# Optimization experiments

Hardware: AMD Instinct MI355X
Metric: run time of the kernel (lower is better)

Reference implementation:

```python
import jax, jax.numpy as jnp
import numpy as np


def setup_inputs() -> dict:
    key = jax.random.key(0)
    k1, k2, k3 = jax.random.split(key, 3)
    bs, S, d, C = 2, 196, 512, 1006
    imgFeaturemap = jax.random.normal(k1, (bs, S, d), dtype=jnp.float32)
    wordFeatures = jax.random.normal(k2, (C, d), dtype=jnp.float32)
    fc3_w = jax.random.normal(k3, (d, d), dtype=jnp.float32) * 0.02
    fc3_b = jnp.zeros((d,), dtype=jnp.float32)
    return {"imgFeaturemap": imgFeaturemap, "wordFeatures": wordFeatures,
            "fc3_w": fc3_w, "fc3_b": fc3_b}


def reference(imgFeaturemap, wordFeatures, fc3_w, fc3_b):
    # imgFeaturemap: (bs, S, d); wordFeatures: (C, d)
    # Broadcast multiply + tanh: (bs, S, C, d)
    t = jnp.tanh(imgFeaturemap[:, :, None, :] * wordFeatures[None, None, :, :])
    # Per-row Linear (PyTorch Linear: x @ W^T + b)
    feat = jnp.einsum('bscd,ed->bsce', t, fc3_w) + fc3_b
    # Softmax over spatial axis S (axis=1), independently per (class, channel)
    coef = jax.nn.softmax(feat, axis=1)
    # Softmax-weighted spatial pooling per class: (bs, C, d)
    semanticFeature = jnp.einsum('bsd,bscd->bcd', imgFeaturemap, coef)
    return semanticFeature
```

## Files before the change

### kernel.cpp

```cpp
#include <hip/hip_runtime.h>

using half8   = __attribute__((ext_vector_type(8))) _Float16;
using floatx4 = __attribute__((ext_vector_type(4))) float;

namespace {
constexpr int S = 196, D = 512, C = 1006;
constexpr int CB  = 8;
constexpr int TPB = 768;
constexpr int RS  = 64;
constexpr int NPASS  = 25;
constexpr int NCHUNK = 200;
constexpr float KTANH = 2.885390082f;
constexpr float LOG2E = 1.44269504f;


__device__ __forceinline__ int sw_off(int row, int seg) {
    return row * RS + ((seg ^ (row & 7)) << 3);
}

__device__ __forceinline__ void gload16(const _Float16* g, _Float16* l) {
    __builtin_amdgcn_global_load_lds(
        (const __attribute__((address_space(1))) unsigned int*)g,
        (__attribute__((address_space(3))) unsigned int*)l, 16, 0, 0);
}

__device__ __forceinline__ _Float16 tanh_ps(float y) {
    float e = __builtin_amdgcn_exp2f(y);
    return (_Float16)(1.0f - 2.0f * __builtin_amdgcn_rcpf(e + 1.0f));
}

__global__ void prep_w16sw(const float* __restrict__ fw, _Float16* __restrict__ W16sw) {
    int id = blockIdx.x * blockDim.x + threadIdx.x;
    int kki = id >> 12;
    int r   = (id >> 3) & 511;
    int j   = id & 7;
    const float* src = fw + (size_t)r * D + kki * 64 + j * 8;
    floatx4 v0 = *(const floatx4*)src;
    floatx4 v1 = *(const floatx4*)(src + 4);
    half8 h;
    h[0] = (_Float16)(v0[0] * LOG2E); h[1] = (_Float16)(v0[1] * LOG2E);
    h[2] = (_Float16)(v0[2] * LOG2E); h[3] = (_Float16)(v0[3] * LOG2E);
    h[4] = (_Float16)(v1[0] * LOG2E); h[5] = (_Float16)(v1[1] * LOG2E);
    h[6] = (_Float16)(v1[2] * LOG2E); h[7] = (_Float16)(v1[3] * LOG2E);
    *(half8*)&W16sw[((size_t)kki << 15) + r * RS + ((j ^ (r & 7)) << 3)] = h;
}

__global__ __launch_bounds__(TPB, 3) void semdec_mfma(
    const float* __restrict__ img, const float* __restrict__ word,
    const _Float16* __restrict__ W16sw, float* __restrict__ out)
{
    __shared__ __align__(16) _Float16 Wc[2][512 * RS];
    __shared__ __align__(16) _Float16 Tc[2][64 * RS];

    const int ct = blockIdx.x;
    const int b  = blockIdx.y;
    const int tid  = threadIdx.x;
    const int lane = tid & 63;
    const int wv   = tid >> 6;
    const int c0   = ct * CB;
    const float* imgB = img + (size_t)b * S * D;

    if (wv >= 8) {
        const int tidT = tid - 512;
        const int sT   = tidT >> 5;
        const int ciT  = (tidT >> 2) & 7;
        const int ksl  = tidT & 3;
        const int rowT = sT * 8 + ciT;
        int cgT = c0 + ciT; if (cgT > C - 1) cgT = C - 1;
        const float* wordT = word + (size_t)cgT * D + ksl * 16;
        const int seg0 = ksl * 2;
        const int off0 = sw_off(rowT, seg0);
        const int off1 = sw_off(rowT, seg0 + 1);

        #pragma unroll
        for (int it = 0; it < 16; ++it) {
            int o = (it * 256 + tidT) * 8;
            gload16(W16sw + o, &Wc[0][o]);
        }
        {
            const float* ip = &imgB[(size_t)sT * D + ksl * 16];
            floatx4 iv[4], wz[4];
            #pragma unroll
            for (int j = 0; j < 4; ++j) {
                iv[j] = *(const floatx4*)(ip + j * 4);
                wz[j] = *(const floatx4*)(wordT + j * 4) * KTANH;
            }
            half8 t0, t1;
            #pragma unroll
            for (int j = 0; j < 8; ++j) {
                t0[j] = tanh_ps(iv[j >> 2][j & 3] * wz[j >> 2][j & 3]);
                t1[j] = tanh_ps(iv[2 + (j >> 2)][j & 3] * wz[2 + (j >> 2)][j & 3]);
            }
            *(half8*)&Tc[0][off0] = t0;
            *(half8*)&Tc[0][off1] = t1;
        }

        for (int lin = 0; lin < NCHUNK; ++lin) {
            __syncthreads();
            const int tl = lin + 1;
            if (tl < NCHUNK) {
                const int pn = tl & 1;
                const _Float16* wg = W16sw + ((size_t)(tl & 7) << 15);
                #pragma unroll
                for (int it = 0; it < 16; ++it) {
                    int o = (it * 256 + tidT) * 8;
                    gload16(wg + o, &Wc[pn][o]);
                }
                const int tkk = tl & 7;
                int srow = (tl >> 3) * 8 + sT; if (srow > S - 1) srow = S - 1;
                const float* ip = &imgB[(size_t)srow * D + tkk * 64 + ksl * 16];
                floatx4 iv[4], wz[4];
                #pragma unroll
                for (int j = 0; j < 4; ++j) {
                    iv[j] = *(const floatx4*)(ip + j * 4);
                    wz[j] = *(const floatx4*)(wordT + tkk * 64 + j * 4) * KTANH;
                }
                half8 t0, t1;
                #pragma unroll
                for (int j = 0; j < 8; ++j) {
                    t0[j] = tanh_ps(iv[j >> 2][j & 3] * wz[j >> 2][j & 3]);
                    t1[j] = tanh_ps(iv[2 + (j >> 2)][j & 3] * wz[2 + (j >> 2)][j & 3]);
                }
                *(half8*)&Tc[pn][off0] = t0;
                *(half8*)&Tc[pn][off1] = t1;
            }
        }
    } else {
        const int l15  = lane & 15;
        const int quad = lane >> 4;

        floatx4 lacc[4], aacc[4];
        #pragma unroll
        for (int ej = 0; ej < 4; ++ej) {
            lacc[ej] = (floatx4){0.f,0.f,0.f,0.f};
            aacc[ej] = (floatx4){0.f,0.f,0.f,0.f};
        }

        for (int pr = 0; pr < NPASS; ++pr) {
            floatx4 acc[4][4];
            #pragma unroll
            for (int sp = 0; sp < 4; ++sp)
                #pragma unroll
                for (int ej = 0; ej < 4; ++ej)
                    acc[sp][ej] = (floatx4){0.f,0.f,0.f,0.f};

            for (int kk = 0; kk < 8; ++kk) {
                __syncthreads();
                const int p = kk & 1;
                const _Float16* Wp = Wc[p];
                const _Float16* Tp = Tc[p];

                {
                    half8 bf[4], af[4];
                    #pragma unroll
                    for (int ej = 0; ej < 4; ++ej)
                        bf[ej] = *(const half8*)&Wp[sw_off(wv * 64 + ej * 16 + l15, quad)];
                    #pragma unroll
                    for (int sp = 0; sp < 4; ++sp)
                        af[sp] = *(const half8*)&Tp[sw_off(sp * 16 + l15, quad)];
                    __builtin_amdgcn_s_setprio(1);
                    #pragma unroll
                    for (int sp = 0; sp < 4; ++sp)
                        #pragma unroll
                        for (int ej = 0; ej < 4; ++ej)
                            acc[sp][ej] = __builtin_amdgcn_mfma_f32_16x16x32_f16(
                                af[sp], bf[ej], acc[sp][ej], 0, 0, 0);
                    __builtin_amdgcn_s_setprio(0);
                }
                {
                    half8 bf[4], af[4];
                    #pragma unroll
                    for (int ej = 0; ej < 4; ++ej)
                        bf[ej] = *(const half8*)&Wp[sw_off(wv * 64 + ej * 16 + l15, 4 + quad)];
                    #pragma unroll
                    for (int sp = 0; sp < 4; ++sp)
                        af[sp] = *(const half8*)&Tp[sw_off(sp * 16 + l15, 4 + quad)];
                    __builtin_amdgcn_s_setprio(1);
                    #pragma unroll
                    for (int sp = 0; sp < 4; ++sp)
                        #pragma unroll
                        for (int ej = 0; ej < 4; ++ej)
                            acc[sp][ej] = __builtin_amdgcn_mfma_f32_16x16x32_f16(
                                af[sp], bf[ej], acc[sp][ej], 0, 0, 0);
                    __builtin_amdgcn_s_setprio(0);
                }
            }

            const int s0 = pr * 8;
            #pragma unroll
            for (int sp = 0; sp < 4; ++sp) {
                const int srow = s0 + sp * 2 + (quad >> 1);
                if (srow < S) {
                    #pragma unroll
                    for (int ej = 0; ej < 4; ++ej) {
                        float ie = imgB[(size_t)srow * D + wv * 64 + ej * 16 + l15];
                        #pragma unroll
                        for (int r = 0; r < 4; ++r) {
                            float ev = __builtin_amdgcn_exp2f(acc[sp][ej][r]);
                            lacc[ej][r] += ev;
                            aacc[ej][r] += ie * ev;
                        }
                    }
                }
            }
        }

        #pragma unroll
        for (int ej = 0; ej < 4; ++ej)
            #pragma unroll
            for (int r = 0; r < 4; ++r) {
                float lv = lacc[ej][r], av = aacc[ej][r];
                lacc[ej][r] = lv + __shfl_xor(lv, 32);
                aacc[ej][r] = av + __shfl_xor(av, 32);
            }

        if (quad < 2) {
            #pragma unroll
            for (int r = 0; r < 4; ++r) {
                const int cg = c0 + quad * 4 + r;
                if (cg < C) {
                    #pragma unroll
                    for (int ej = 0; ej < 4; ++ej) {
                        const int eg = wv * 64 + ej * 16 + l15;
                        out[((size_t)b * C + cg) * D + eg] = aacc[ej][r] / lacc[ej][r];
                    }
                }
            }
        }
    }
}

}

extern "C" void kernel_launch(void* const* d_in, const int* in_sizes, int n_in,
                              void* d_out, int out_size, void* d_ws, size_t ws_size,
                              hipStream_t stream) {
    const float* img  = (const float*)d_in[0];
    const float* word = (const float*)d_in[1];
    const float* fw   = (const float*)d_in[2];
    float* out = (float*)d_out;

    _Float16* W16sw = (_Float16*)d_ws;

    hipLaunchKernelGGL(prep_w16sw, dim3(128), dim3(256), 0, stream, fw, W16sw);
    hipLaunchKernelGGL(semdec_mfma, dim3(126, 2), dim3(TPB), 0, stream,
                       img, word, W16sw, out);
}
```

Before: 354.0 us.

## Stagger per-block k-chunk order and prefetch producer operands one chunk ahead

Producer waves now start at a block-dependent k-chunk offset so concurrent blocks fetch different W slices, spreading L2/HBM traffic. They also load the img and word values for chunk t+2 into registers while computing tanh for chunk t+1, hiding global-load latency behind the tanh work. This costs extra registers in the producer waves and relies on the k-sum being order-independent.

```diff
diff --git a/kernel.cpp b/kernel.cpp
--- a/kernel.cpp
+++ b/kernel.cpp
@@ -54,6 +54,8 @@
 
     const int ct = blockIdx.x;
     const int b  = blockIdx.y;
+    const int bid  = blockIdx.y * gridDim.x + blockIdx.x;
+    const int phase = (bid >> 3) & 7;
     const int tid  = threadIdx.x;
     const int lane = tid & 63;
     const int wv   = tid >> 6;
@@ -72,54 +74,76 @@
         const int off0 = sw_off(rowT, seg0);
         const int off1 = sw_off(rowT, seg0 + 1);
 
-        #pragma unroll
-        for (int it = 0; it < 16; ++it) {
-            int o = (it * 256 + tidT) * 8;
-            gload16(W16sw + o, &Wc[0][o]);
-        }
         {
-            const float* ip = &imgB[(size_t)sT * D + ksl * 16];
-            floatx4 iv[4], wz[4];
+            const _Float16* wg = W16sw + ((size_t)phase << 15);
+            #pragma unroll
+            for (int it = 0; it < 16; ++it) {
+                int o = (it * 256 + tidT) * 8;
+                gload16(wg + o, &Wc[0][o]);
+            }
+        }
+        {
+            const float* ip = &imgB[(size_t)sT * D + phase * 64 + ksl * 16];
+            floatx4 iv0[4], wz0[4];
             #pragma unroll
             for (int j = 0; j < 4; ++j) {
-                iv[j] = *(const floatx4*)(ip + j * 4);
-                wz[j] = *(const floatx4*)(wordT + j * 4) * KTANH;
+                iv0[j] = *(const floatx4*)(ip + j * 4);
+                wz0[j] = *(const floatx4*)(wordT + phase * 64 + j * 4) * KTANH;
             }
             half8 t0, t1;
             #pragma unroll
             for (int j = 0; j < 8; ++j) {
-                t0[j] = tanh_ps(iv[j >> 2][j & 3] * wz[j >> 2][j & 3]);
-                t1[j] = tanh_ps(iv[2 + (j >> 2)][j & 3] * wz[2 + (j >> 2)][j & 3]);
+                t0[j] = tanh_ps(iv0[j >> 2][j & 3] * wz0[j >> 2][j & 3]);
+                t1[j] = tanh_ps(iv0[2 + (j >> 2)][j & 3] * wz0[2 + (j >> 2)][j & 3]);
             }
             *(half8*)&Tc[0][off0] = t0;
             *(half8*)&Tc[0][off1] = t1;
         }
+        floatx4 ivB[4], wzB[4];
+        {
+            const int kn1 = (1 + phase) & 7;
+            const float* ip = &imgB[(size_t)sT * D + kn1 * 64 + ksl * 16];
+            #pragma unroll
+            for (int j = 0; j < 4; ++j) {
+                ivB[j] = *(const floatx4*)(ip + j * 4);
+                wzB[j] = *(const floatx4*)(wordT + kn1 * 64 + j * 4);
+            }
+        }
 
         for (int lin = 0; lin < NCHUNK; ++lin) {
             __syncthreads();
+            floatx4 ivA[4], wzA[4];
+            #pragma unroll
+            for (int j = 0; j < 4; ++j) { ivA[j] = ivB[j]; wzA[j] = wzB[j]; }
+
             const int tl = lin + 1;
             if (tl < NCHUNK) {
                 const int pn = tl & 1;
-                const _Float16* wg = W16sw + ((size_t)(tl & 7) << 15);
+                const int kn = ((tl & 7) + phase) & 7;
+                const _Float16* wg = W16sw + ((size_t)kn << 15);
                 #pragma unroll
                 for (int it = 0; it < 16; ++it) {
                     int o = (it * 256 + tidT) * 8;
                     gload16(wg + o, &Wc[pn][o]);
                 }
-                const int tkk = tl & 7;
-                int srow = (tl >> 3) * 8 + sT; if (srow > S - 1) srow = S - 1;
-                const float* ip = &imgB[(size_t)srow * D + tkk * 64 + ksl * 16];
-                floatx4 iv[4], wz[4];
-                #pragma unroll
-                for (int j = 0; j < 4; ++j) {
-                    iv[j] = *(const floatx4*)(ip + j * 4);
-                    wz[j] = *(const floatx4*)(wordT + tkk * 64 + j * 4) * KTANH;
+                if (tl + 1 < NCHUNK) {
+                    const int t2  = tl + 1;
+                    const int kn2 = ((t2 & 7) + phase) & 7;
+                    int srow = (t2 >> 3) * 8 + sT; if (srow > S - 1) srow = S - 1;
+                    const float* ip = &imgB[(size_t)srow * D + kn2 * 64 + ksl * 16];
+                    #pragma unroll
+                    for (int j = 0; j < 4; ++j) {
+                        ivB[j] = *(const floatx4*)(ip + j * 4);
+                        wzB[j] = *(const floatx4*)(wordT + kn2 * 64 + j * 4);
+                    }
                 }
                 half8 t0, t1;
                 #pragma unroll
+                for (int j = 0; j < 4; ++j) wzA[j] *= KTANH;
+                #pragma unroll
                 for (int j = 0; j < 8; ++j) {
-                    t0[j] = tanh_ps(iv[j >> 2][j & 3] * wz[j >> 2][j & 3]);
-                    t1[j] = tanh_ps(iv[2 + (j >> 2)][j & 3] * wz[2 + (j >> 2)][j & 3]);
+                    t0[j] = tanh_ps(ivA[j >> 2][j & 3] * wzA[j >> 2][j & 3]);
+                    t1[j] = tanh_ps(ivA[2 + (j >> 2)][j & 3] * wzA[2 + (j >> 2)][j & 3]);
                 }
                 *(half8*)&Tc[pn][off0] = t0;
                 *(half8*)&Tc[pn][off1] = t1;
```

After: 335.7 us. 1.05x faster.
